# Kernel optimization log

Measured on AMD Instinct MI355X. Metric: run time of the kernel, lower is better.

The kernel has to match this reference:

```python
import jax, jax.numpy as jnp
import numpy as np

# Dims: B batch, C=P channels (features per pixel), H*W=N pixels, M ELM models, Q=1 hidden units
M, Q, B, C, H, W_SP = 4, 1, 32, 1024, 28, 28
P = C
N = H * W_SP
EPS = 1e-10


def _lcg_weights(m, n, seed):
    """Deterministic LCG pseudo-random weights, z-score standardized (ELM_AE init)."""
    L = m * n
    a, b, c = L + 2, L + 3, float(L) ** 2
    v = np.zeros(L, dtype=np.float64)
    v[0] = seed + 1.0
    for i in range(1, L):
        v[i] = (a * v[i - 1] + b) % c
    v = (v - v.mean()) / (v.std() + EPS)
    return v.reshape(m, n).astype(np.float32)


def setup_inputs() -> dict:
    key = jax.random.key(0)
    x = jax.random.normal(key, (B, C, H, W_SP), dtype=jnp.float32)
    # One Q x P random input-weight matrix per ELM model, seed = model * (Q * P)
    Wm = jnp.stack([jnp.asarray(_lcg_weights(Q, P, model * (Q * P))) for model in range(M)])  # [M, Q, P]
    return {"x": x, "Wm": Wm}


def reference(x, Wm):
    b, c, h, w = x.shape
    # _norm('l2', ...): per-channel L2 normalization over (h, w), as F.normalize(dim=(1,2))
    norms = jnp.linalg.norm(x.reshape(b, c, h * w), axis=-1)[:, :, None, None]  # [B, C, 1, 1]
    xn = x / jnp.maximum(norms, EPS)
    X = xn.reshape(b, c, h * w)  # meta activation map per sample: [B, P, N]
    # ELM-AE hidden layer, batched over (sample, model): g = sigmoid(W @ X)
    G = jax.nn.sigmoid(jnp.einsum('mqp,bpn->bmqn', Wm, X))  # [B, M, Q, N]
    # fit_AE: output weights beta = pinv(g^T) @ X^T  -> [Q, P]
    pinvGt = jnp.linalg.pinv(jnp.swapaxes(G, -1, -2))       # [B, M, Q, N]
    beta = jnp.einsum('bmqn,bpn->bmqp', pinvGt, X)          # [B, M, Q, P]
    # sum over the M models; Q == 1 so flatten (Q, P) -> Q*P features
    feats = beta.sum(axis=1).reshape(b, -1)                 # [B, Q*P]
    return jnp.nan_to_num(feats)
```

## Files before the change

### kernel.cpp

```cpp
#include <hip/hip_runtime.h>
#include <math.h>

#define BATCH 32
#define CH    1024
#define NPix  784
#define MMOD  4
#define NZB   32
#define CPB   2
#define PPC   16
#define K1B   256
#define NF4   196
#define T2    832

__device__ __forceinline__ float wave_reduce(float s) {
    #pragma unroll
    for (int off = 32; off; off >>= 1) s += __shfl_down(s, off, 64);
    return s;
}

__device__ __forceinline__ float dpp_wave_sum(float v) {
    int x;
    x = __builtin_amdgcn_update_dpp(0, __builtin_bit_cast(int, v), 0x111, 0xf, 0xf, true);
    v += __builtin_bit_cast(float, x);
    x = __builtin_amdgcn_update_dpp(0, __builtin_bit_cast(int, v), 0x112, 0xf, 0xf, true);
    v += __builtin_bit_cast(float, x);
    x = __builtin_amdgcn_update_dpp(0, __builtin_bit_cast(int, v), 0x114, 0xf, 0xf, true);
    v += __builtin_bit_cast(float, x);
    x = __builtin_amdgcn_update_dpp(0, __builtin_bit_cast(int, v), 0x118, 0xf, 0xf, true);
    v += __builtin_bit_cast(float, x);
    x = __builtin_amdgcn_update_dpp(0, __builtin_bit_cast(int, v), 0x142, 0xa, 0xf, true);
    v += __builtin_bit_cast(float, x);
    x = __builtin_amdgcn_update_dpp(0, __builtin_bit_cast(int, v), 0x143, 0xc, 0xf, true);
    v += __builtin_bit_cast(float, x);
    return v;
}

__global__ __launch_bounds__(K1B) void k_nz(const float* __restrict__ x,
                                            const float* __restrict__ Wm,
                                            float* __restrict__ inv_norm,
                                            float* __restrict__ zpart) {
    __shared__ float sq_l[PPC][4];
    __shared__ float4 wl4[PPC];
    const int blk = blockIdx.x;
    const int b   = blk >> 5;
    const int pcg = blk & (NZB - 1);
    const int t = threadIdx.x;
    const int wv = t >> 6, lane = t & 63;
    const bool act = (t < NF4);
    const int tt = act ? t : 0;

    float4 a0 = {0,0,0,0}, a1 = {0,0,0,0}, a2 = {0,0,0,0}, a3 = {0,0,0,0};

    #pragma unroll
    for (int c = 0; c < CPB; c++) {
        const int ch0 = pcg * (CPB * PPC) + c * PPC;
        const float4* xb4 = (const float4*)(x + ((size_t)b * CH + ch0) * NPix);

        float4 xv[PPC];
        #pragma unroll
        for (int pp = 0; pp < PPC; pp++) xv[pp] = xb4[pp * NF4 + tt];

        #pragma unroll
        for (int pp = 0; pp < PPC; pp++) {
            float4 v = xv[pp];
            float s = act ? (v.x*v.x + v.y*v.y + v.z*v.z + v.w*v.w) : 0.f;
            s = dpp_wave_sum(s);
            if (lane == 63) sq_l[pp][wv] = s;
        }
        __syncthreads();

        if (t < PPC) {
            const float s = sq_l[t][0] + sq_l[t][1] + sq_l[t][2] + sq_l[t][3];
            const float inv = 1.f / fmaxf(sqrtf(s), 1e-10f);
            const int p = ch0 + t;
            inv_norm[b * CH + p] = inv;
            float4 w4;
            w4.x = Wm[0 * CH + p] * inv;
            w4.y = Wm[1 * CH + p] * inv;
            w4.z = Wm[2 * CH + p] * inv;
            w4.w = Wm[3 * CH + p] * inv;
            wl4[t] = w4;
        }
        __syncthreads();

        if (act) {
            #pragma unroll
            for (int pp = 0; pp < PPC; pp++) {
                const float4 w = wl4[pp];
                const float4 v = xv[pp];
                a0.x += w.x*v.x; a0.y += w.x*v.y; a0.z += w.x*v.z; a0.w += w.x*v.w;
                a1.x += w.y*v.x; a1.y += w.y*v.y; a1.z += w.y*v.z; a1.w += w.y*v.w;
                a2.x += w.z*v.x; a2.y += w.z*v.y; a2.z += w.z*v.z; a2.w += w.z*v.w;
                a3.x += w.w*v.x; a3.y += w.w*v.y; a3.z += w.w*v.z; a3.w += w.w*v.w;
            }
        }
    }

    if (act) {
        float4* zp = (float4*)(zpart + ((size_t)blk * MMOD) * NPix);
        zp[0 * NF4 + t] = a0;
        zp[1 * NF4 + t] = a1;
        zp[2 * NF4 + t] = a2;
        zp[3 * NF4 + t] = a3;
    }
}

__global__ __launch_bounds__(T2) void k_gh(const float* __restrict__ zpart,
                                           float* __restrict__ g_out,
                                           float* __restrict__ s2g) {
    __shared__ float red[13];
    const int blk = blockIdx.x;
    const int b = blk >> 2;
    const int m = blk & 3;
    const int t = threadIdx.x;
    const int wv = t >> 6, lane = t & 63;
    const bool act = (t < NPix);

    float z = 0.f;
    if (act) {
        #pragma unroll
        for (int pc = 0; pc < NZB; pc++)
            z += zpart[(((size_t)(b * NZB + pc)) * MMOD + m) * NPix + t];
    }
    const float g = act ? 1.f / (1.f + expf(-z)) : 0.f;
    float s = wave_reduce(g * g);
    if (lane == 0) red[wv] = s;
    __syncthreads();
    if (t == 0) {
        float ss = 0.f;
        #pragma unroll
        for (int w = 0; w < 13; w++) ss += red[w];
        s2g[blk] = fmaxf(ss, 1e-30f);
    }
    if (act) g_out[(size_t)blk * NPix + t] = g;
}

__global__ __launch_bounds__(256) void k_h(const float* __restrict__ g_out,
                                           const float* __restrict__ s2g,
                                           float* __restrict__ h) {
    const int b = blockIdx.x >> 2;
    const int q = blockIdx.x & 3;
    const int t = threadIdx.x;
    if (t < NF4) {
        const int n = q * NF4 + t;
        float hv = 0.f;
        #pragma unroll
        for (int m = 0; m < MMOD; m++)
            hv += g_out[(size_t)(b * MMOD + m) * NPix + n] / s2g[b * MMOD + m];
        h[(size_t)b * NPix + n] = hv;
    }
}

__global__ __launch_bounds__(256) void k_out(const float* __restrict__ x,
                                             const float* __restrict__ h,
                                             const float* __restrict__ inv_norm,
                                             float* __restrict__ out) {
    const int r = blockIdx.x * 4 + (threadIdx.x >> 6);
    const int lane = threadIdx.x & 63;
    const int b = r >> 10;
    const float4* x4 = (const float4*)(x + (size_t)r * NPix);
    const float4* h4 = (const float4*)(h + (size_t)b * NPix);
    float s = 0.f;
    #pragma unroll
    for (int i = 0; i < 3; i++) {
        float4 xv = x4[i * 64 + lane];
        float4 hv = h4[i * 64 + lane];
        s += xv.x*hv.x + xv.y*hv.y + xv.z*hv.z + xv.w*hv.w;
    }
    if (lane < 4) {
        float4 xv = x4[192 + lane];
        float4 hv = h4[192 + lane];
        s += xv.x*hv.x + xv.y*hv.y + xv.z*hv.z + xv.w*hv.w;
    }
    s = wave_reduce(s);
    if (lane == 0) {
        float v = s * inv_norm[r];
        if (!(v == v)) v = 0.f;
        v = fminf(fmaxf(v, -3.402823466e+38f), 3.402823466e+38f);
        out[r] = v;
    }
}

extern "C" void kernel_launch(void* const* d_in, const int* in_sizes, int n_in,
                              void* d_out, int out_size, void* d_ws, size_t ws_size,
                              hipStream_t stream) {
    const float* x  = (const float*)d_in[0];
    const float* Wm = (const float*)d_in[1];
    float* out = (float*)d_out;
    float* wsf = (float*)d_ws;

    float* inv_norm = wsf;
    float* zpart    = inv_norm + BATCH * CH;
    float* g_out    = zpart + (size_t)BATCH * NZB * MMOD * NPix;
    float* s2g      = g_out + (size_t)BATCH * MMOD * NPix;
    float* h        = s2g + BATCH * MMOD;

    k_nz<<<BATCH * NZB, K1B, 0, stream>>>(x, Wm, inv_norm, zpart);
    k_gh<<<BATCH * MMOD, T2, 0, stream>>>(zpart, g_out, s2g);
    k_h<<<BATCH * MMOD, 256, 0, stream>>>(g_out, s2g, h);
    k_out<<<BATCH * CH / 4, 256, 0, stream>>>(x, h, inv_norm, out);
}
```

Before: 175.5 us.

## Load all 32 channels at once in k_nz and fuse k_gh with k_h

k_nz now loads all 32 channels per block into registers in a single pass, with one pair of barriers instead of two sequential 16-channel chunks. This raises memory-level parallelism but greatly increases register pressure (32 float4 per thread), which may lower occupancy or spill. k_gh now handles all four models per batch in one block and computes h directly. This removes the k_h launch and the g_out/s2g round trip through global memory, at the cost of fewer blocks (32 instead of 128) for the reduction.

```diff
diff --git a/kernel.cpp b/kernel.cpp
--- a/kernel.cpp
+++ b/kernel.cpp
@@ -6,8 +6,7 @@
 #define NPix  784
 #define MMOD  4
 #define NZB   32
-#define CPB   2
-#define PPC   16
+#define CPB   32
 #define K1B   256
 #define NF4   196
 #define T2    832
@@ -39,8 +38,8 @@
                                             const float* __restrict__ Wm,
                                             float* __restrict__ inv_norm,
                                             float* __restrict__ zpart) {
-    __shared__ float sq_l[PPC][4];
-    __shared__ float4 wl4[PPC];
+    __shared__ float sq_l[CPB][4];
+    __shared__ float4 wl4[CPB];
     const int blk = blockIdx.x;
     const int b   = blk >> 5;
     const int pcg = blk & (NZB - 1);
@@ -48,55 +47,47 @@
     const int wv = t >> 6, lane = t & 63;
     const bool act = (t < NF4);
     const int tt = act ? t : 0;
+    const int ch0 = pcg * CPB;
+    const float4* xb4 = (const float4*)(x + ((size_t)b * CH + ch0) * NPix);
 
-    float4 a0 = {0,0,0,0}, a1 = {0,0,0,0}, a2 = {0,0,0,0}, a3 = {0,0,0,0};
+    float4 xv[CPB];
+    #pragma unroll
+    for (int pp = 0; pp < CPB; pp++) xv[pp] = xb4[pp * NF4 + tt];
 
     #pragma unroll
-    for (int c = 0; c < CPB; c++) {
-        const int ch0 = pcg * (CPB * PPC) + c * PPC;
-        const float4* xb4 = (const float4*)(x + ((size_t)b * CH + ch0) * NPix);
+    for (int pp = 0; pp < CPB; pp++) {
+        float4 v = xv[pp];
+        float s = act ? (v.x*v.x + v.y*v.y + v.z*v.z + v.w*v.w) : 0.f;
+        s = dpp_wave_sum(s);
+        if (lane == 63) sq_l[pp][wv] = s;
+    }
+    __syncthreads();
 
-        float4 xv[PPC];
-        #pragma unroll
-        for (int pp = 0; pp < PPC; pp++) xv[pp] = xb4[pp * NF4 + tt];
-
-        #pragma unroll
-        for (int pp = 0; pp < PPC; pp++) {
-            float4 v = xv[pp];
-            float s = act ? (v.x*v.x + v.y*v.y + v.z*v.z + v.w*v.w) : 0.f;
-            s = dpp_wave_sum(s);
-            if (lane == 63) sq_l[pp][wv] = s;
-        }
-        __syncthreads();
-
-        if (t < PPC) {
-            const float s = sq_l[t][0] + sq_l[t][1] + sq_l[t][2] + sq_l[t][3];
-            const float inv = 1.f / fmaxf(sqrtf(s), 1e-10f);
-            const int p = ch0 + t;
-            inv_norm[b * CH + p] = inv;
-            float4 w4;
-            w4.x = Wm[0 * CH + p] * inv;
-            w4.y = Wm[1 * CH + p] * inv;
-            w4.z = Wm[2 * CH + p] * inv;
-            w4.w = Wm[3 * CH + p] * inv;
-            wl4[t] = w4;
-        }
-        __syncthreads();
-
-        if (act) {
-            #pragma unroll
-            for (int pp = 0; pp < PPC; pp++) {
-                const float4 w = wl4[pp];
-                const float4 v = xv[pp];
-                a0.x += w.x*v.x; a0.y += w.x*v.y; a0.z += w.x*v.z; a0.w += w.x*v.w;
-                a1.x += w.y*v.x; a1.y += w.y*v.y; a1.z += w.y*v.z; a1.w += w.y*v.w;
-                a2.x += w.z*v.x; a2.y += w.z*v.y; a2.z += w.z*v.z; a2.w += w.z*v.w;
-                a3.x += w.w*v.x; a3.y += w.w*v.y; a3.z += w.w*v.z; a3.w += w.w*v.w;
-            }
-        }
+    if (t < CPB) {
+        const float s = sq_l[t][0] + sq_l[t][1] + sq_l[t][2] + sq_l[t][3];
+        const float inv = 1.f / fmaxf(sqrtf(s), 1e-10f);
+        const int p = ch0 + t;
+        inv_norm[b * CH + p] = inv;
+        float4 w4;
+        w4.x = Wm[0 * CH + p] * inv;
+        w4.y = Wm[1 * CH + p] * inv;
+        w4.z = Wm[2 * CH + p] * inv;
+        w4.w = Wm[3 * CH + p] * inv;
+        wl4[t] = w4;
     }
+    __syncthreads();
 
     if (act) {
+        float4 a0 = {0,0,0,0}, a1 = {0,0,0,0}, a2 = {0,0,0,0}, a3 = {0,0,0,0};
+        #pragma unroll
+        for (int pp = 0; pp < CPB; pp++) {
+            const float4 w = wl4[pp];
+            const float4 v = xv[pp];
+            a0.x += w.x*v.x; a0.y += w.x*v.y; a0.z += w.x*v.z; a0.w += w.x*v.w;
+            a1.x += w.y*v.x; a1.y += w.y*v.y; a1.z += w.y*v.z; a1.w += w.y*v.w;
+            a2.x += w.z*v.x; a2.y += w.z*v.y; a2.z += w.z*v.z; a2.w += w.z*v.w;
+            a3.x += w.w*v.x; a3.y += w.w*v.y; a3.z += w.w*v.z; a3.w += w.w*v.w;
+        }
         float4* zp = (float4*)(zpart + ((size_t)blk * MMOD) * NPix);
         zp[0 * NF4 + t] = a0;
         zp[1 * NF4 + t] = a1;
@@ -106,48 +97,45 @@
 }
 
 __global__ __launch_bounds__(T2) void k_gh(const float* __restrict__ zpart,
-                                           float* __restrict__ g_out,
-                                           float* __restrict__ s2g) {
-    __shared__ float red[13];
-    const int blk = blockIdx.x;
-    const int b = blk >> 2;
-    const int m = blk & 3;
+                                           float* __restrict__ h) {
+    __shared__ float red[MMOD][13];
+    __shared__ float rs2[MMOD];
+    const int b = blockIdx.x;
     const int t = threadIdx.x;
     const int wv = t >> 6, lane = t & 63;
     const bool act = (t < NPix);
 
-    float z = 0.f;
+    float zm[MMOD] = {0.f, 0.f, 0.f, 0.f};
     if (act) {
         #pragma unroll
-        for (int pc = 0; pc < NZB; pc++)
-            z += zpart[(((size_t)(b * NZB + pc)) * MMOD + m) * NPix + t];
+        for (int pc = 0; pc < NZB; pc++) {
+            const float* zp = zpart + (((size_t)(b * NZB + pc)) * MMOD) * NPix + t;
+            zm[0] += zp[0 * NPix];
+            zm[1] += zp[1 * NPix];
+            zm[2] += zp[2 * NPix];
+            zm[3] += zp[3 * NPix];
+        }
     }
-    const float g = act ? 1.f / (1.f + expf(-z)) : 0.f;
-    float s = wave_reduce(g * g);
-    if (lane == 0) red[wv] = s;
+    float gm[MMOD];
+    #pragma unroll
+    for (int m = 0; m < MMOD; m++) {
+        gm[m] = act ? 1.f / (1.f + expf(-zm[m])) : 0.f;
+        float s = wave_reduce(gm[m] * gm[m]);
+        if (lane == 0) red[m][wv] = s;
+    }
     __syncthreads();
-    if (t == 0) {
+    if (t < MMOD) {
         float ss = 0.f;
         #pragma unroll
-        for (int w = 0; w < 13; w++) ss += red[w];
-        s2g[blk] = fmaxf(ss, 1e-30f);
+        for (int w = 0; w < 13; w++) ss += red[t][w];
+        rs2[t] = fmaxf(ss, 1e-30f);
     }
-    if (act) g_out[(size_t)blk * NPix + t] = g;
-}
-
-__global__ __launch_bounds__(256) void k_h(const float* __restrict__ g_out,
-                                           const float* __restrict__ s2g,
-                                           float* __restrict__ h) {
-    const int b = blockIdx.x >> 2;
-    const int q = blockIdx.x & 3;
-    const int t = threadIdx.x;
-    if (t < NF4) {
-        const int n = q * NF4 + t;
+    __syncthreads();
+    if (act) {
         float hv = 0.f;
         #pragma unroll
-        for (int m = 0; m < MMOD; m++)
-            hv += g_out[(size_t)(b * MMOD + m) * NPix + n] / s2g[b * MMOD + m];
-        h[(size_t)b * NPix + n] = hv;
+        for (int m = 0; m < MMOD; m++) hv += gm[m] / rs2[m];
+        h[(size_t)b * NPix + t] = hv;
     }
 }
 
@@ -191,12 +179,9 @@
 
     float* inv_norm = wsf;
     float* zpart    = inv_norm + BATCH * CH;
-    float* g_out    = zpart + (size_t)BATCH * NZB * MMOD * NPix;
-    float* s2g      = g_out + (size_t)BATCH * MMOD * NPix;
-    float* h        = s2g + BATCH * MMOD;
+    float* h        = zpart + (size_t)BATCH * NZB * MMOD * NPix;
 
     k_nz<<<BATCH * NZB, K1B, 0, stream>>>(x, Wm, inv_norm, zpart);
-    k_gh<<<BATCH * MMOD, T2, 0, stream>>>(zpart, g_out, s2g);
-    k_h<<<BATCH * MMOD, 256, 0, stream>>>(g_out, s2g, h);
+    k_gh<<<BATCH, T2, 0, stream>>>(zpart, h);
     k_out<<<BATCH * CH / 4, 256, 0, stream>>>(x, h, inv_norm, out);
 }
```

Result: no change. 177.7 us (+1.2%).
